# Kernel tuning notes

Measured on AMD Instinct MI355X. Metric: run time of the kernel, lower is better.

The kernel has to match this reference:

```python
import jax, jax.numpy as jnp
import numpy as np

TOKEN_NUMS = 206
IGNORE_IDX = -100
HALF_TOKEN = float((TOKEN_NUMS - 4) / 2)  # 101.0

B, S = 256, 682
T = 3 * S + 2  # 2048


def setup_inputs() -> dict:
    key = jax.random.key(0)
    k1, k2, k3, k4 = jax.random.split(key, 4)
    pred = jax.random.normal(k1, (B, T, TOKEN_NUMS), dtype=jnp.float32)
    gt_acc = jax.random.uniform(k2, (B, S), dtype=jnp.float32)
    gt_steer = jax.random.uniform(k3, (B, S), dtype=jnp.float32)
    gt_reverse = jax.random.randint(k4, (B, S), 0, 2, dtype=jnp.int64)
    return {"pred": pred, "gt_acc": gt_acc, "gt_steer": gt_steer, "gt_reverse": gt_reverse}


def _smooth_l1(pred, target):
    d = pred - target
    ad = jnp.abs(d)
    return jnp.mean(jnp.where(ad < 1.0, 0.5 * d * d, ad - 0.5))


def reference(pred, gt_acc, gt_steer, gt_reverse):
    pred_control = pred[:, :-2, :]
    acc_logits = pred_control[:, 0::3, :]    # [B, S, V]
    steer_logits = pred_control[:, 1::3, :]  # [B, S, V]
    rev_logits = pred_control[:, 2::3, :]    # [B, S, V]

    # softmax followed by argmax == argmax of logits (softmax is monotonic)
    acc_idx = jnp.argmax(acc_logits, axis=-1).reshape(-1).astype(jnp.float32)
    # vectorized detokenize_acc: if token > half: t/half - 1 else -(t/half - 1)
    pred_acc = jnp.where(acc_idx > HALF_TOKEN, acc_idx / HALF_TOKEN - 1.0,
                         1.0 - acc_idx / HALF_TOKEN)
    acc_val_loss = _smooth_l1(pred_acc, gt_acc.reshape(-1))

    steer_idx = jnp.argmax(steer_logits, axis=-1).reshape(-1).astype(jnp.float32)
    pred_steer = steer_idx / HALF_TOKEN - 1.0  # detokenize_steer
    steer_val_loss = _smooth_l1(pred_steer, gt_steer.reshape(-1))

    acc_steer_val_loss = acc_val_loss + steer_val_loss

    # reverse branch: sum softmax prob mass over the two token ranges per row
    rev_probs = jax.nn.softmax(rev_logits.reshape(-1, TOKEN_NUMS), axis=-1)
    p_no_reverse = jnp.sum(rev_probs[:, :101], axis=-1)
    p_reverse = jnp.sum(rev_probs[:, 101:], axis=-1)
    two_class = jnp.stack([p_no_reverse, p_reverse], axis=-1)  # [N, 2]
    # nn.CrossEntropyLoss applies log_softmax to its input (here: probabilities)
    logp = jax.nn.log_softmax(two_class, axis=-1)
    gt = gt_reverse.reshape(-1)
    valid = gt != IGNORE_IDX
    gt_safe = jnp.where(valid, gt, 0)
    nll = -jnp.take_along_axis(logp, gt_safe[:, None], axis=1)[:, 0]
    reverse_val_loss = jnp.sum(jnp.where(valid, nll, 0.0)) / jnp.maximum(
        jnp.sum(valid.astype(jnp.float32)), 1.0)

    return acc_steer_val_loss, reverse_val_loss
```

## Files before the change

kernel.cpp:

```cpp
#include <hip/hip_runtime.h>
#include <cstddef>

namespace {
constexpr int TOK   = 206;
constexpr int NROWS = 256 * 682;
constexpr int R     = 8;
constexpr int NGRP  = NROWS / R;
constexpr int GRID  = 2048;
constexpr int LROW2 = 310;
constexpr int LDSF2 = R * LROW2 + 16;
constexpr int NSLOT = 64;
}

typedef float f32x4 __attribute__((ext_vector_type(4)));

__global__ __launch_bounds__(256) void cvl_main(
    const float* __restrict__ pred,
    const float* __restrict__ gt_acc,
    const float* __restrict__ gt_steer,
    const int*  __restrict__ gt_rev,
    double* __restrict__ ws)
{
    __shared__ alignas(16) double lds2[LDSF2];

    const int tid = threadIdx.x;
    const int sr  = tid >> 5;
    const int sc  = tid & 31;
    const int lane = tid & 63;
    const int wid  = tid >> 6;
    const int l32  = lane & 31;

    float accS = 0.f, steerS = 0.f, revS = 0.f, cntS = 0.f;

    f32x4 v[5];
    double tl = 0.0;
    int   gtN; float gaN, gsN;
    auto load_group = [&](int g) {
        const int row = g * R + sr;
        const unsigned bb = (unsigned)row / 682u;
        const float* base = pred + (size_t)(3u * (unsigned)row + 2u * bb) * TOK;
        #pragma unroll
        for (int k = 0; k < 4; ++k)
            v[k] = __builtin_nontemporal_load((const f32x4*)base + sc + 32 * k);
        if (sc < 26)
            v[4] = __builtin_nontemporal_load((const f32x4*)base + sc + 128);
        if (sc == 31)
            tl = __builtin_nontemporal_load((const double*)(base + 616));
        gtN = gt_rev[row];
        gaN = gt_acc[row];
        gsN = gt_steer[row];
    };

    int g = blockIdx.x;
    if (g < NGRP) load_group(g);

    while (g < NGRP) {
        f32x4* lrow4 = (f32x4*)(lds2 + sr * LROW2);
        #pragma unroll
        for (int k = 0; k < 4; ++k) lrow4[sc + 32 * k] = v[k];
        if (sc < 26) lrow4[sc + 128] = v[4];
        if (sc == 31) lds2[sr * LROW2 + 308] = tl;
        const int   gt = gtN;
        const float ga = gaN;
        const float gs = gsN;
        __syncthreads();

        const int gn = g + GRID;
        if (gn < NGRP) load_group(gn);

        const double* rp = &lds2[sr * LROW2];
        float2 q[10];
        #pragma unroll
        for (int k = 0; k < 10; ++k)
            q[k] = __builtin_bit_cast(float2, rp[l32 + 32 * k]);

        float aM = q[0].x; int aI = 2 * l32;
        if (q[0].y > aM) { aM = q[0].y; aI = 2 * l32 + 1; }
        #pragma unroll
        for (int k = 1; k <= 2; ++k) {
            const int t = 2 * (l32 + 32 * k);
            if (q[k].x > aM) { aM = q[k].x; aI = t; }
            if (q[k].y > aM) { aM = q[k].y; aI = t + 1; }
        }
        float sM = -INFINITY; int sI = 0;
        {
            const int i2 = l32 + 96;
            if (l32 < 7) {
                if (q[3].x > aM) { aM = q[3].x; aI = 2 * i2; }
                if (q[3].y > aM) { aM = q[3].y; aI = 2 * i2 + 1; }
            } else {
                sM = q[3].x; sI = 2 * i2 - 206;
                if (q[3].y > sM) { sM = q[3].y; sI = 2 * i2 - 205; }
            }
        }
        #pragma unroll
        for (int k = 4; k <= 5; ++k) {
            const int st = 2 * (l32 + 32 * k) - 206;
            if (q[k].x > sM) { sM = q[k].x; sI = st; }
            if (q[k].y > sM) { sM = q[k].y; sI = st + 1; }
        }
        float lo = 0.f, hi = 0.f;
        {
            if (l32 < 14) {
                const int st = 2 * (l32 + 192) - 206;
                if (q[6].x > sM) { sM = q[6].x; sI = st; }
                if (q[6].y > sM) { sM = q[6].y; sI = st + 1; }
            } else {
                lo += __expf(q[6].x) + __expf(q[6].y);
            }
        }
        lo += __expf(q[7].x) + __expf(q[7].y);
        {
            const float ex = __expf(q[8].x), ey = __expf(q[8].y);
            if (l32 == 0) lo += ex; else hi += ex;
            hi += ey;
        }
        if (l32 < 21) hi += __expf(q[9].x) + __expf(q[9].y);

        #pragma unroll
        for (int off = 16; off >= 1; off >>= 1) {
            const float av = __shfl_xor(aM, off);
            const int   ai = __shfl_xor(aI, off);
            if (av > aM) { aM = av; aI = ai; }
            const float sv = __shfl_xor(sM, off);
            const int   si = __shfl_xor(sI, off);
            if (sv > sM) { sM = sv; sI = si; }
            lo += __shfl_xor(lo, off);
            hi += __shfl_xor(hi, off);
        }

        {
            const float Z    = lo + hi;
            const float pno  = lo / Z;
            const float prv  = hi / Z;
            const float ai_f = (float)aI;
            const float si_f = (float)sI;
            const float pa   = (ai_f > 101.f) ? (ai_f * (1.f / 101.f) - 1.f)
                                              : (1.f - ai_f * (1.f / 101.f));
            const float ps   = si_f * (1.f / 101.f) - 1.f;
            const float da   = pa - ga;
            const float dsv  = ps - gs;
            const float ada  = fabsf(da), ads = fabsf(dsv);
            accS   += (ada < 1.f) ? 0.5f * da * da   : ada - 0.5f;
            steerS += (ads < 1.f) ? 0.5f * dsv * dsv : ads - 0.5f;
            if (gt != -100) {
                const float m2 = fmaxf(pno, prv);
                revS += m2 + __logf(__expf(pno - m2) + __expf(prv - m2))
                        - ((gt == 0) ? pno : prv);
                cntS += 1.f;
            }
        }
        __syncthreads();
        g = gn;
    }

    accS   += __shfl_xor(accS, 32);
    steerS += __shfl_xor(steerS, 32);
    revS   += __shfl_xor(revS, 32);
    cntS   += __shfl_xor(cntS, 32);

    __shared__ float red[4][4];
    if (lane == 0) {
        red[wid][0] = accS; red[wid][1] = steerS;
        red[wid][2] = revS; red[wid][3] = cntS;
    }
    __syncthreads();
    if (tid == 0) {
        double a = 0, st = 0, rr = 0, c = 0;
        for (int w = 0; w < 4; ++w) {
            a += red[w][0]; st += red[w][1]; rr += red[w][2]; c += red[w][3];
        }
        double* slot = ws + (size_t)(blockIdx.x & (NSLOT - 1)) * 4;
        atomicAdd(slot + 0, a);
        atomicAdd(slot + 1, st);
        atomicAdd(slot + 2, rr);
        atomicAdd(slot + 3, c);
    }
}

__global__ void cvl_init(double* __restrict__ ws) {
    const int i = blockIdx.x * blockDim.x + threadIdx.x;
    if (i < NSLOT * 4) ws[i] = 0.0;
}

__global__ void cvl_final(const double* __restrict__ ws, float* __restrict__ out) {
    const int t = threadIdx.x;
    double a = ws[4 * t], st = ws[4 * t + 1], r = ws[4 * t + 2], c = ws[4 * t + 3];
    #pragma unroll
    for (int off = 32; off >= 1; off >>= 1) {
        a  += __shfl_xor(a,  off);
        st += __shfl_xor(st, off);
        r  += __shfl_xor(r,  off);
        c  += __shfl_xor(c,  off);
    }
    if (t == 0) {
        const double n = (double)NROWS;
        out[0] = (float)(a / n + st / n);
        out[1] = (float)(r / fmax(c, 1.0));
    }
}

extern "C" void kernel_launch(void* const* d_in, const int* in_sizes, int n_in,
                              void* d_out, int out_size, void* d_ws, size_t ws_size,
                              hipStream_t stream) {
    const float* pred     = (const float*)d_in[0];
    const float* gt_acc   = (const float*)d_in[1];
    const float* gt_steer = (const float*)d_in[2];
    const int*   gt_rev   = (const int*)d_in[3];
    double* ws  = (double*)d_ws;
    float*  out = (float*)d_out;

    cvl_init<<<1, 256, 0, stream>>>(ws);
    cvl_main<<<GRID, 256, 0, stream>>>(pred, gt_acc, gt_steer, gt_rev, ws);
    cvl_final<<<1, 64, 0, stream>>>(ws, out);
}
```

Measured before the change: 82.37 us.

## Make each wavefront own a row pair and drop block barriers

Work is now split per wavefront rather than per block. Each wave stages two rows, one per half-wave, into its own private LDS region and processes them, so both block-wide __syncthreads calls are removed. The grid is also resized to 1984 blocks, with the stride counted in waves. This is meant to stop waves in a block from stalling on one another and to let each wave run its own load pipeline, at the cost of relying on in-order LDS access within a wavefront for correctness.

```diff
diff --git a/kernel.cpp b/kernel.cpp
--- a/kernel.cpp
+++ b/kernel.cpp
@@ -4,11 +4,11 @@
 namespace {
 constexpr int TOK   = 206;
 constexpr int NROWS = 256 * 682;
-constexpr int R     = 8;
-constexpr int NGRP  = NROWS / R;
-constexpr int GRID  = 2048;
+constexpr int NPAIR = NROWS / 2;
+constexpr int GRID  = 1984;
+constexpr int NWAVE = GRID * 4;
 constexpr int LROW2 = 310;
-constexpr int LDSF2 = R * LROW2 + 16;
+constexpr int LDSF2 = 8 * LROW2 + 16;
 constexpr int NSLOT = 64;
 }
 
@@ -23,20 +23,22 @@
 {
     __shared__ alignas(16) double lds2[LDSF2];
 
-    const int tid = threadIdx.x;
-    const int sr  = tid >> 5;
-    const int sc  = tid & 31;
+    const int tid  = threadIdx.x;
     const int lane = tid & 63;
     const int wid  = tid >> 6;
     const int l32  = lane & 31;
+    const int h    = lane >> 5;
+    const int sr   = tid >> 5;
+    const int sc   = l32;
+    double* myrow  = lds2 + sr * LROW2;
 
     float accS = 0.f, steerS = 0.f, revS = 0.f, cntS = 0.f;
 
     f32x4 v[5];
     double tl = 0.0;
     int   gtN; float gaN, gsN;
-    auto load_group = [&](int g) {
-        const int row = g * R + sr;
+    auto load_pair = [&](int p) {
+        const int row = 2 * p + h;
         const unsigned bb = (unsigned)row / 682u;
         const float* base = pred + (size_t)(3u * (unsigned)row + 2u * bb) * TOK;
         #pragma unroll
@@ -51,28 +53,26 @@
         gsN = gt_steer[row];
     };
 
-    int g = blockIdx.x;
-    if (g < NGRP) load_group(g);
-
-    while (g < NGRP) {
-        f32x4* lrow4 = (f32x4*)(lds2 + sr * LROW2);
+    int p = blockIdx.x * 4 + wid;
+    load_pair(p);
+
+    while (p < NPAIR) {
+        f32x4* lrow4 = (f32x4*)myrow;
         #pragma unroll
         for (int k = 0; k < 4; ++k) lrow4[sc + 32 * k] = v[k];
         if (sc < 26) lrow4[sc + 128] = v[4];
-        if (sc == 31) lds2[sr * LROW2 + 308] = tl;
+        if (sc == 31) myrow[308] = tl;
         const int   gt = gtN;
         const float ga = gaN;
         const float gs = gsN;
-        __syncthreads();
-
-        const int gn = g + GRID;
-        if (gn < NGRP) load_group(gn);
-
-        const double* rp = &lds2[sr * LROW2];
+
+        const int pn = p + NWAVE;
+        if (pn < NPAIR) load_pair(pn);
+
         float2 q[10];
         #pragma unroll
         for (int k = 0; k < 10; ++k)
-            q[k] = __builtin_bit_cast(float2, rp[l32 + 32 * k]);
+            q[k] = __builtin_bit_cast(float2, myrow[l32 + 32 * k]);
 
         float aM = q[0].x; int aI = 2 * l32;
         if (q[0].y > aM) { aM = q[0].y; aI = 2 * l32 + 1; }
@@ -150,8 +150,7 @@
                 cntS += 1.f;
             }
         }
-        __syncthreads();
-        g = gn;
+        p = pn;
     }
 
     accS   += __shfl_xor(accS, 32);
```

New measurement: 82.61 us. About the same (+0.3%).
